# Optimization experiments

Hardware: AMD Instinct MI355X
Metric: run time of the kernel (lower is better)

## Reference

```python
import jax, jax.numpy as jnp
import numpy as np

R = 3            # window radius -> (2R+1)^2 = 49 neighbors
N = 128          # grid side, n
K = 131          # 3 + 64 + 64 channels
C = 21           # num_classes
B = 2            # batch
W = (2 * R + 1) ** 2


def setup_inputs() -> dict:
    key = jax.random.key(0)
    k1, k2, k3, k4 = jax.random.split(key, 4)
    return {
        "intergrated": jax.random.normal(k1, (B, K, N, N), jnp.float32),
        "x2": jax.random.normal(k2, (B, C, N * N), jnp.float32),
        "sel_mask": jax.random.randint(k3, (B, N, N), 0, 2).astype(jnp.int32),
        "conv_parameter": jax.random.uniform(k4, (K,), jnp.float32),
    }


def _shifts(x, r):
    """Gather (2r+1)^2 shifted copies: x [..., n, n] -> [..., n, n, W].
    Entry w=(di,dj) holds x[i+di-r, j+dj-r] (zero-padded out of bounds)."""
    n = x.shape[-1]
    pad = [(0, 0)] * (x.ndim - 2) + [(r, r), (r, r)]
    xp = jnp.pad(x, pad)
    cols = [xp[..., di:di + n, dj:dj + n]
            for di in range(2 * r + 1) for dj in range(2 * r + 1)]
    return jnp.stack(cols, axis=-1)


def _rwn_single(feats, x2b, maskb, conv_parameter):
    """feats [K,n,n], x2b [C,n^2], maskb [n,n] int -> y [n^2, C]."""
    n = feats.shape[-1]
    m = maskb.astype(feats.dtype)            # sampled-pixel indicator
    xm = feats * m                            # sparse-sampled features [K,n,n]
    nbr = _shifts(xm, R)                      # [K,n,n,W] neighbor values
    valid = _shifts(jnp.ones((n, n), feats.dtype), R) > 0  # [n,n,W] in-bounds
    # per-channel windowed L1 distance, exp, per-pixel normalization (softmax
    # of +distance over the valid window, as in the original code)
    d = jnp.abs(xm[..., None] - nbr)          # [K,n,n,W]
    e = jnp.where(valid[None], jnp.exp(d), 0.0)
    a = e / e.sum(axis=-1, keepdims=True)     # rows sum to 1 per channel
    # W = sum_k conv_parameter[k] * a_k, rows only for selected pixels
    A = jnp.einsum('k,kijw->ijw', conv_parameter, a) * m[..., None]  # [n,n,W]
    # y[q,c] = sum_p W[p,q] * x2[p,c]  (W^T @ x2^T, per original col/row swap)
    feat = x2b.reshape(C, n, n)
    msg = A[None] * feat[..., None]           # [C,n,n,W]
    ypad = jnp.zeros((C, n + 2 * R, n + 2 * R), feats.dtype)
    w = 0
    for di in range(2 * R + 1):
        for dj in range(2 * R + 1):
            ypad = ypad.at[:, di:di + n, dj:dj + n].add(msg[..., w])
            w += 1
    y = ypad[:, R:R + n, R:R + n].reshape(C, n * n)
    return y.T                                 # [n^2, C]


def reference(intergrated, x2, sel_mask, conv_parameter):
    f = lambda fe, xb, mb: _rwn_single(fe, xb, mb, conv_parameter)
    return jax.vmap(f)(intergrated, x2, sel_mask)  # [B, n^2, C]
```

## Files before the change

kernel.cpp:

```cpp
#include <hip/hip_runtime.h>
#include <hip/hip_fp16.h>

#define R_ 3
#define D_ 7
#define W_ 49
#define N_ 128
#define K_ 131
#define C_ 21
#define B_ 2
#define NN (N_ * N_)
#define TI_ 8
#define TJ_ 16
#define PROWS (TI_ + 2 * R_)
#define PCOLS (TJ_ + 2 * R_)
#define PSTR 24
#define NELEM (PROWS * PCOLS)
#define LDSP (PROWS * PSTR + 8)
#define KC 8
#define KCHUNK ((K_ + KC - 1) / KC)
#define HCELLS (PROWS * PCOLS)

typedef __fp16 h2 __attribute__((ext_vector_type(2)));

__global__ __launch_bounds__(256) void rwn_affinity(
    const float* __restrict__ feats,
    const int*   __restrict__ mask,
    const float* __restrict__ cp,
    float* __restrict__ Aout)
{
    __shared__ float2 patch2[LDSP];

    const int tile = blockIdx.x;
    const int kc   = blockIdx.y;
    const int b    = blockIdx.z;
    const int tr = tile >> 3, tc = tile & 7;
    const int ti0 = tr * TI_, tj0 = tc * TJ_;

    const int tid = threadIdx.x;
    const int pix = tid >> 1;
    const int h   = tid & 1;
    const int ti = pix >> 4;
    const int tj = pix & 15;
    const int gi = ti0 + ti, gj = tj0 + tj;

    const float LOG2E = 1.4426950408889634f;
    int   soff[2];
    float swt[2];
    float ozw[2];
    int   slds[2];
    #pragma unroll
    for (int r = 0; r < 2; ++r) {
        int e = tid + r * 256;
        bool act = (e < NELEM);
        int pr = e / PCOLS, pc = e - pr * PCOLS;
        int mi = ti0 + pr - R_, mj = tj0 + pc - R_;
        bool inb = act && mi >= 0 && mi < N_ && mj >= 0 && mj < N_;
        int cmi = mi < 0 ? 0 : (mi > N_ - 1 ? N_ - 1 : mi);
        int cmj = mj < 0 ? 0 : (mj > N_ - 1 ? N_ - 1 : mj);
        soff[r] = cmi * N_ + cmj;
        swt[r]  = inb ? ((float)mask[b * NN + soff[r]] * LOG2E) : 0.f;
        ozw[r]  = inb ? 1.f : 0.f;
        slds[r] = act ? (pr * PSTR + pc) : (PROWS * PSTR + 4);
    }

    const float ph = h ? 0.f : 1.f;
    const int cbase = ti * PSTR + tj;
    const int bh = cbase + h;

    h2 Aacc[14];
    #pragma unroll
    for (int i = 0; i < 14; ++i) Aacc[i] = (h2){(__fp16)0.f, (__fp16)0.f};

    const int k0 = kc * KCHUNK;
    const int k1 = (k0 + KCHUNK < K_) ? (k0 + KCHUNK) : K_;
    const float* fb = feats + (size_t)b * K_ * NN;

    for (int e = tid; e < LDSP; e += 256) patch2[e] = make_float2(0.f, 0.f);

    const float* fk0 = fb + (size_t)k0 * NN;
    float pre0 = fk0[soff[0]] * swt[0];
    float pre1 = fk0[soff[1]] * swt[1];

    __syncthreads();

    for (int k = k0; k < k1; ++k) {
        patch2[slds[0]] = make_float2(ozw[0] * exp2f(pre0), ozw[0] * exp2f(-pre0));
        patch2[slds[1]] = make_float2(ozw[1] * exp2f(pre1), ozw[1] * exp2f(-pre1));
        float n0 = 0.f, n1 = 0.f;
        if (k + 1 < k1) {
            const float* fn = fb + (size_t)(k + 1) * NN;
            n0 = fn[soff[0]] * swt[0];
            n1 = fn[soff[1]] * swt[1];
        }
        __syncthreads();

        const float2 cpair = patch2[cbase + R_ * PSTR + R_];
        h2 ex[14];
        float dsum = 0.f;
        #pragma unroll
        for (int u = 0; u < D_; ++u) {
            #pragma unroll
            for (int m = 0; m < 2; ++m) {
                const float2 np0 = patch2[bh + u * PSTR + 4 * m];
                const float2 np1 = patch2[bh + u * PSTR + 4 * m + 2];
                float t0 = fmaxf(cpair.x * np0.y, np0.x * cpair.y);
                float t1 = fmaxf(cpair.x * np1.y, np1.x * cpair.y);
                if (m == 1) t1 *= ph;
                dsum += t0;
                dsum += t1;
                ex[u * 2 + m] = __builtin_amdgcn_cvt_pkrtz(t0, t1);
            }
        }
        const float denom = dsum + __shfl_xor(dsum, 1, 64);
        const float scale = cp[k] * __frcp_rn(denom);
        const h2 s2 = __builtin_amdgcn_cvt_pkrtz(scale, scale);
        #pragma unroll
        for (int m = 0; m < 14; ++m) Aacc[m] = ex[m] * s2 + Aacc[m];
        __syncthreads();

        pre0 = n0; pre1 = n1;
    }

    if (mask[b * NN + gi * N_ + gj] != 0) {
        const int pixg = gi * N_ + gj;
        float* ab = Aout + (size_t)b * W_ * NN + h * NN + pixg;
        #pragma unroll
        for (int u = 0; u < D_; ++u) {
            #pragma unroll
            for (int m = 0; m < 2; ++m) {
                const h2 tv = Aacc[u * 2 + m];
                atomicAdd(ab + (u * D_ + 4 * m) * NN, (float)tv[0]);
                if (h == 0 || m < 1)
                    atomicAdd(ab + (u * D_ + 4 * m + 2) * NN, (float)tv[1]);
            }
        }
    }
}

__global__ __launch_bounds__(512) void rwn_gather(
    const float* __restrict__ Aarr,
    const float* __restrict__ x2,
    float* __restrict__ out)
{
    __shared__ float x2h[C_ * HCELLS];

    const int tile = blockIdx.x;
    const int b    = blockIdx.y;
    const int tr = tile >> 3, tc = tile & 7;
    const int gi0 = tr * TI_, gj0 = tc * TJ_;

    const int tid = threadIdx.x;

    const float* xb = x2 + (size_t)b * C_ * NN;
    for (int e = tid; e < C_ * HCELLS; e += 512) {
        const int c = e / HCELLS, cell = e - c * HCELLS;
        const int pr = cell / PCOLS, pc = cell - pr * PCOLS;
        const int mi = gi0 + pr - R_, mj = gj0 + pc - R_;
        const bool inb = (mi >= 0 && mi < N_ && mj >= 0 && mj < N_);
        const int cmi = mi < 0 ? 0 : (mi > N_ - 1 ? N_ - 1 : mi);
        const int cmj = mj < 0 ? 0 : (mj > N_ - 1 ? N_ - 1 : mj);
        x2h[e] = inb ? xb[c * NN + cmi * N_ + cmj] : 0.f;
    }
    __syncthreads();

    const int h = tid & 3;
    const int q = tid >> 2;
    const int qi = q >> 4, qj = q & 15;
    const int gi = gi0 + qi, gj = gj0 + qj;
    const float* Ab = Aarr + (size_t)b * W_ * NN;

    float av[13];
    int   cells[13];
    #pragma unroll
    for (int idx = 0; idx < 13; ++idx) {
        int w = h + 4 * idx;
        const float valid = (w < W_) ? 1.f : 0.f;
        if (w >= W_) w = W_ - 1;
        const int u = w / D_, v = w - u * D_;
        const int pi = gi + R_ - u, pj = gj + R_ - v;
        const int cmi = pi < 0 ? 0 : (pi > N_ - 1 ? N_ - 1 : pi);
        const int cmj = pj < 0 ? 0 : (pj > N_ - 1 ? N_ - 1 : pj);
        av[idx]    = valid * Ab[(size_t)w * NN + cmi * N_ + cmj];
        cells[idx] = (qi + 2 * R_ - u) * PCOLS + (qj + 2 * R_ - v);
    }

    float acc[C_];
    #pragma unroll
    for (int c = 0; c < C_; ++c) acc[c] = 0.f;
    #pragma unroll
    for (int idx = 0; idx < 13; ++idx) {
        const float a = av[idx];
        const float* xc = x2h + cells[idx];
        #pragma unroll
        for (int c = 0; c < C_; ++c)
            acc[c] += a * xc[c * HCELLS];
    }

    #pragma unroll
    for (int c = 0; c < C_; ++c) {
        acc[c] += __shfl_xor(acc[c], 1, 64);
        acc[c] += __shfl_xor(acc[c], 2, 64);
    }

    __syncthreads();
    if (h == 0) {
        float* os = x2h + q * C_;
        #pragma unroll
        for (int c = 0; c < C_; ++c) os[c] = acc[c];
    }
    __syncthreads();
    for (int e = tid; e < TI_ * TJ_ * C_; e += 512) {
        const int qq = e / C_, cc = e - qq * C_;
        const int gq = (gi0 + (qq >> 4)) * N_ + gj0 + (qq & 15);
        out[((size_t)b * NN + gq) * C_ + cc] = x2h[e];
    }
}

extern "C" void kernel_launch(void* const* d_in, const int* in_sizes, int n_in,
                              void* d_out, int out_size, void* d_ws, size_t ws_size,
                              hipStream_t stream) {
    const float* feats = (const float*)d_in[0];
    const float* x2    = (const float*)d_in[1];
    const int*   mask  = (const int*)d_in[2];
    const float* cp    = (const float*)d_in[3];
    float* out = (float*)d_out;

    float* Aarr = (float*)d_ws;
    const size_t Abytes = (size_t)B_ * W_ * NN * sizeof(float);

    (void)hipMemsetAsync(Aarr, 0, Abytes, stream);

    dim3 gridA(128, KC, B_);
    rwn_affinity<<<gridA, 256, 0, stream>>>(feats, mask, cp, Aarr);

    dim3 gridG(128, B_);
    rwn_gather<<<gridG, 512, 0, stream>>>(Aarr, x2, out);
}
```

Baseline: 145.6 us.

## Store patch exps as packed fp16 and compute window affinities with packed half math

The shared-memory patch now holds exp(+x) and exp(-x) as one packed fp16 word instead of a float2. The per-window max/product math runs on packed half2 vectors, and the sum uses fdot2. The window-to-thread split also changes: each half-thread now covers contiguous column pairs, which changes the atomic write indices to match. The goal is lower LDS traffic and fewer ALU ops, at the cost of fp16 range and precision for the exp values, which could overflow for large feature magnitudes.

```diff
diff --git a/kernel.cpp b/kernel.cpp
--- a/kernel.cpp
+++ b/kernel.cpp
@@ -22,13 +22,25 @@
 
 typedef __fp16 h2 __attribute__((ext_vector_type(2)));
 
+static __device__ __forceinline__ unsigned h2u(h2 x) { return __builtin_bit_cast(unsigned, x); }
+static __device__ __forceinline__ h2 u2h(unsigned x) { return __builtin_bit_cast(h2, x); }
+
+#if defined(__has_builtin)
+#if __has_builtin(__builtin_amdgcn_fdot2)
+#define FDOT2(a, b, c) __builtin_amdgcn_fdot2((a), (b), (c), false)
+#endif
+#endif
+#ifndef FDOT2
+#define FDOT2(a, b, c) ((c) + (float)(a)[0] * (float)(b)[0] + (float)(a)[1] * (float)(b)[1])
+#endif
+
 __global__ __launch_bounds__(256) void rwn_affinity(
     const float* __restrict__ feats,
     const int*   __restrict__ mask,
     const float* __restrict__ cp,
     float* __restrict__ Aout)
 {
-    __shared__ float2 patch2[LDSP];
+    __shared__ unsigned patchw[LDSP];
 
     const int tile = blockIdx.x;
     const int kc   = blockIdx.y;
@@ -63,9 +75,11 @@
         slds[r] = act ? (pr * PSTR + pc) : (PROWS * PSTR + 4);
     }
 
-    const float ph = h ? 0.f : 1.f;
-    const int cbase = ti * PSTR + tj;
-    const int bh = cbase + h;
+    const h2 ph2 = h ? (h2){(__fp16)1.f, (__fp16)0.f}
+                     : (h2){(__fp16)1.f, (__fp16)1.f};
+    const h2 one2 = (h2){(__fp16)1.f, (__fp16)1.f};
+    const int cbase = (ti + R_) * PSTR + (tj + R_);
+    const int bh = ti * PSTR + tj + 4 * h;
 
     h2 Aacc[14];
     #pragma unroll
@@ -75,7 +89,7 @@
     const int k1 = (k0 + KCHUNK < K_) ? (k0 + KCHUNK) : K_;
     const float* fb = feats + (size_t)b * K_ * NN;
 
-    for (int e = tid; e < LDSP; e += 256) patch2[e] = make_float2(0.f, 0.f);
+    for (int e = tid; e < LDSP; e += 256) patchw[e] = 0u;
 
     const float* fk0 = fb + (size_t)k0 * NN;
     float pre0 = fk0[soff[0]] * swt[0];
@@ -84,8 +98,10 @@
     __syncthreads();
 
     for (int k = k0; k < k1; ++k) {
-        patch2[slds[0]] = make_float2(ozw[0] * exp2f(pre0), ozw[0] * exp2f(-pre0));
-        patch2[slds[1]] = make_float2(ozw[1] * exp2f(pre1), ozw[1] * exp2f(-pre1));
+        patchw[slds[0]] = h2u(__builtin_amdgcn_cvt_pkrtz(ozw[0] * exp2f(pre0),
+                                                         ozw[0] * exp2f(-pre0)));
+        patchw[slds[1]] = h2u(__builtin_amdgcn_cvt_pkrtz(ozw[1] * exp2f(pre1),
+                                                         ozw[1] * exp2f(-pre1)));
         float n0 = 0.f, n1 = 0.f;
         if (k + 1 < k1) {
             const float* fn = fb + (size_t)(k + 1) * NN;
@@ -94,22 +110,30 @@
         }
         __syncthreads();
 
-        const float2 cpair = patch2[cbase + R_ * PSTR + R_];
+        const unsigned cw = patchw[cbase];
+        const h2 cE2 = u2h(__builtin_amdgcn_perm(cw, cw, 0x01000100u));
+        const h2 cI2 = u2h(__builtin_amdgcn_perm(cw, cw, 0x03020302u));
+
         h2 ex[14];
         float dsum = 0.f;
         #pragma unroll
         for (int u = 0; u < D_; ++u) {
-            #pragma unroll
-            for (int m = 0; m < 2; ++m) {
-                const float2 np0 = patch2[bh + u * PSTR + 4 * m];
-                const float2 np1 = patch2[bh + u * PSTR + 4 * m + 2];
-                float t0 = fmaxf(cpair.x * np0.y, np0.x * cpair.y);
-                float t1 = fmaxf(cpair.x * np1.y, np1.x * cpair.y);
-                if (m == 1) t1 *= ph;
-                dsum += t0;
-                dsum += t1;
-                ex[u * 2 + m] = __builtin_amdgcn_cvt_pkrtz(t0, t1);
-            }
+            const int rb = bh + u * PSTR;
+            const unsigned w0 = patchw[rb];
+            const unsigned w1 = patchw[rb + 1];
+            const unsigned w2 = patchw[rb + 2];
+            const unsigned w3 = patchw[rb + 3];
+            const h2 E01 = u2h(__builtin_amdgcn_perm(w1, w0, 0x05040100u));
+            const h2 I01 = u2h(__builtin_amdgcn_perm(w1, w0, 0x07060302u));
+            const h2 E23 = u2h(__builtin_amdgcn_perm(w3, w2, 0x05040100u));
+            const h2 I23 = u2h(__builtin_amdgcn_perm(w3, w2, 0x07060302u));
+            h2 t01 = __builtin_elementwise_max(cE2 * I01, E01 * cI2);
+            h2 t23 = __builtin_elementwise_max(cE2 * I23, E23 * cI2);
+            t23 = t23 * ph2;
+            dsum = FDOT2(t01, one2, dsum);
+            dsum = FDOT2(t23, one2, dsum);
+            ex[u * 2]     = t01;
+            ex[u * 2 + 1] = t23;
         }
         const float denom = dsum + __shfl_xor(dsum, 1, 64);
         const float scale = cp[k] * __frcp_rn(denom);
@@ -123,15 +147,16 @@
 
     if (mask[b * NN + gi * N_ + gj] != 0) {
         const int pixg = gi * N_ + gj;
-        float* ab = Aout + (size_t)b * W_ * NN + h * NN + pixg;
+        float* ab = Aout + (size_t)b * W_ * NN + pixg;
         #pragma unroll
         for (int u = 0; u < D_; ++u) {
             #pragma unroll
             for (int m = 0; m < 2; ++m) {
                 const h2 tv = Aacc[u * 2 + m];
-                atomicAdd(ab + (u * D_ + 4 * m) * NN, (float)tv[0]);
+                const int wbase = u * D_ + 4 * h + 2 * m;
+                atomicAdd(ab + (size_t)wbase * NN, (float)tv[0]);
                 if (h == 0 || m < 1)
-                    atomicAdd(ab + (u * D_ + 4 * m + 2) * NN, (float)tv[1]);
+                    atomicAdd(ab + (size_t)(wbase + 1) * NN, (float)tv[1]);
             }
         }
     }
```

Result: slower. 149.1 us (+2.4%).
